# Kernel tuning notes

Hardware: AMD Instinct MI355X
Metric: run time of the kernel (lower is better)

Reference implementation:

```python
import jax, jax.numpy as jnp
import numpy as np

F = 32          # fmap_size = (256 // 16) * 2
WIN = F // 8 - 1  # window = 3
HID = 160
HID4 = 640
N = 4096
Q = 16


def setup_inputs() -> dict:
    key = jax.random.key(0)
    ks = jax.random.split(key, 24)

    def lin(k, i, o):
        return jax.random.normal(k, (i, o), jnp.float32) * (1.0 / np.sqrt(i))

    return {
        "feature_pos": jax.random.normal(ks[0], (N, Q, HID), jnp.float32),
        "query_embedding": jax.random.normal(ks[1], (N, Q, HID), jnp.float32),
        "attn_matrix": jax.random.normal(ks[2], (N, Q, F * F), jnp.float32),
        "ws1": lin(ks[3], HID, HID4), "bs1": jnp.zeros((HID4,), jnp.float32),
        "ws2": lin(ks[4], HID4, HID4), "bs2": jnp.zeros((HID4,), jnp.float32),
        "ws3": lin(ks[5], HID4, HID4), "bs3": jnp.zeros((HID4,), jnp.float32),
        "ws4": lin(ks[6], HID4, 1), "bs4": jnp.zeros((1,), jnp.float32),
        "wp1": lin(ks[7], HID, HID4), "bp1": jnp.zeros((HID4,), jnp.float32),
        "wp2": lin(ks[8], HID4, HID4), "bp2": jnp.zeros((HID4,), jnp.float32),
        "wp3": lin(ks[9], HID4, HID4), "bp3": jnp.zeros((HID4,), jnp.float32),
        "wp4": lin(ks[10], HID4, 4), "bp4": jnp.zeros((4,), jnp.float32),
    }


def _mlp(x, w1, b1, w2, b2, w3, b3, w4, b4):
    h = jax.nn.relu(x @ w1 + b1)
    h = jax.nn.relu(h @ w2 + b2)
    h = jax.nn.relu(h @ w3 + b3)
    return h @ w4 + b4


def _gauss_blur3(x):
    # torchvision GaussianBlur(3, sigma=1.0): separable 3-tap, reflect padding
    e = np.exp(-0.5)
    k = jnp.asarray([e, 1.0, e], jnp.float32) / np.float32(1.0 + 2.0 * e)
    xp = jnp.pad(x, ((0, 0), (1, 1), (0, 0)), mode="reflect")
    x = k[0] * xp[:, :-2] + k[1] * xp[:, 1:-1] + k[2] * xp[:, 2:]
    xp = jnp.pad(x, ((0, 0), (0, 0), (1, 1)), mode="reflect")
    return k[0] * xp[:, :, :-2] + k[1] * xp[:, :, 1:-1] + k[2] * xp[:, :, 2:]


def _process_attnmap(am):
    # am: [N, F, F]
    n = am.shape[0]
    ab = _gauss_blur3(am)
    ab = (ab - ab.mean(axis=(1, 2), keepdims=True)) / jnp.std(ab, axis=(1, 2), keepdims=True, ddof=1)
    idx = jnp.argmax(ab.reshape(n, -1), axis=1)
    px = (idx % F).astype(jnp.int32)
    py = (idx // F).astype(jnp.int32)
    # vectorized windowed mean of clamped sigmoid (masked instead of per-sample slicing)
    s = jnp.clip(jax.nn.sigmoid(am), 1e-4, 1.0 - 1e-4)
    pos = jnp.arange(F)
    colmask = ((pos[None, :] >= jnp.maximum(0, px - WIN)[:, None]) &
               (pos[None, :] < jnp.minimum(F, px + WIN)[:, None])).astype(s.dtype)  # [N,F]
    rowmask = ((pos[None, :] >= jnp.maximum(0, py - WIN)[:, None]) &
               (pos[None, :] < jnp.minimum(F, py + WIN)[:, None])).astype(s.dtype)
    colsum = s.sum(axis=1)  # [N,F] sum over rows -> per-column totals
    rowsum = s.sum(axis=2)  # [N,F] sum over cols -> per-row totals
    tempx = (colsum * colmask).sum(axis=1) / (F * colmask.sum(axis=1))
    tempy = (rowsum * rowmask).sum(axis=1) / (F * rowmask.sum(axis=1))
    prepos = jnp.stack([px, py], axis=1).astype(jnp.float32)          # [N,2]
    presize = jnp.stack([tempx, tempy], axis=1) * np.float32(F)        # [N,2]
    return prepos, presize


def reference(feature_pos, query_embedding, attn_matrix,
              ws1, bs1, ws2, bs2, ws3, bs3, ws4, bs4,
              wp1, bp1, wp2, bp2, wp3, bp3, wp4, bp4):
    n = query_embedding.shape[0]
    qe = query_embedding.mean(axis=1)   # [N, HID]
    fp = feature_pos.mean(axis=1)       # [N, HID]
    am = attn_matrix.mean(axis=1).reshape(n, F, F)
    score = _mlp(qe, ws1, bs1, ws2, bs2, ws3, bs3, ws4, bs4).reshape(n)
    bbox_info = _mlp(fp, wp1, bp1, wp2, bp2, wp3, bp3, wp4, bp4)  # [N,4]
    sizeoffset = jnp.clip(bbox_info[:, :2], -2.0, 2.0)
    posoffset = jnp.clip(bbox_info[:, 2:], -2.0, 2.0)
    prepos, presize = _process_attnmap(am)
    xy = (prepos + posoffset) / np.float32(F)
    wh = (presize + sizeoffset) / np.float32(F)
    xy = xy - 0.5 * wh  # predict_center
    bbox = jnp.concatenate([xy, wh], axis=1)
    return bbox, score
```

## Files before the change

### kernel.cpp

```cpp
#include <hip/hip_runtime.h>
#include <hip/hip_bf16.h>
#include <stdint.h>

#define HID 160
#define HID4 640
#define FDIM 32
#define NPIX 1024

#define GK0 0.27406862f
#define GK1 0.45186276f

typedef __attribute__((ext_vector_type(8))) short short8;
typedef __attribute__((ext_vector_type(4))) float f32x4;

__device__ __forceinline__ ushort f2b(float f) {
  union { float f; uint32_t u; } v; v.f = f;
  uint32_t u = v.u;
  u += 0x7fffu + ((u >> 16) & 1u);
  return (ushort)(u >> 16);
}
__device__ __forceinline__ float b2f(ushort s) {
  union { uint32_t u; float f; } v; v.u = ((uint32_t)s) << 16;
  return v.f;
}

__device__ __forceinline__ void gload16(const ushort* g, ushort* l) {
  __builtin_amdgcn_global_load_lds(
      (const __attribute__((address_space(1))) void*)g,
      (__attribute__((address_space(3))) void*)l, 16, 0, 0);
}

struct AttnSM {
  float am[FDIM][FDIM + 1];
  float tmp[FDIM][FDIM + 1];
  float bl[FDIM][FDIM + 1];
  float rowsum[FDIM], colsum[FDIM];
  float redv[4];
  int redi[4];
};

union GemmSM {
  struct {
    ushort la[2][4096];
    ushort lb[2][2048];
  } g;
  AttnSM a;
};

union PrepSM {
  float t[32][33];
  AttnSM a;
};

__device__ void attn_block(AttnSM& sm, const float* __restrict__ attn,
                           float* __restrict__ pp, int n) {
  const int tid = threadIdx.x;
  const float* base = attn + (size_t)n * (16 * NPIX);
  float4 a = make_float4(0.f, 0.f, 0.f, 0.f);
#pragma unroll
  for (int q = 0; q < 16; ++q) {
    float4 v = *(const float4*)(base + q * NPIX + tid * 4);
    a.x += v.x; a.y += v.y; a.z += v.z; a.w += v.w;
  }
  {
    const int f0 = tid * 4;
    const int r = f0 >> 5, c = f0 & 31;
    sm.am[r][c + 0] = a.x * 0.0625f;
    sm.am[r][c + 1] = a.y * 0.0625f;
    sm.am[r][c + 2] = a.z * 0.0625f;
    sm.am[r][c + 3] = a.w * 0.0625f;
  }
  __syncthreads();
  for (int f = tid; f < NPIX; f += 256) {
    int r = f >> 5, c = f & 31;
    int rm = (r == 0) ? 1 : r - 1;
    int rp = (r == 31) ? 30 : r + 1;
    sm.tmp[r][c] = GK0 * sm.am[rm][c] + GK1 * sm.am[r][c] + GK0 * sm.am[rp][c];
  }
  __syncthreads();
  for (int f = tid; f < NPIX; f += 256) {
    int r = f >> 5, c = f & 31;
    int cm = (c == 0) ? 1 : c - 1;
    int cp = (c == 31) ? 30 : c + 1;
    sm.bl[r][c] = GK0 * sm.tmp[r][cm] + GK1 * sm.tmp[r][c] + GK0 * sm.tmp[r][cp];
  }
  __syncthreads();
  float bv = -1e30f; int bi = 0;
  for (int f = tid; f < NPIX; f += 256) {
    float v = sm.bl[f >> 5][f & 31];
    if (v > bv || (v == bv && f < bi)) { bv = v; bi = f; }
  }
  for (int off = 32; off > 0; off >>= 1) {
    float ov = __shfl_down(bv, off);
    int oi = __shfl_down(bi, off);
    if (ov > bv || (ov == bv && oi < bi)) { bv = ov; bi = oi; }
  }
  if ((tid & 63) == 0) { sm.redv[tid >> 6] = bv; sm.redi[tid >> 6] = bi; }
  for (int f = tid; f < NPIX; f += 256) {
    int r = f >> 5, c = f & 31;
    float s = 1.f / (1.f + expf(-sm.am[r][c]));
    sm.tmp[r][c] = fminf(fmaxf(s, 1e-4f), 0.9999f);
  }
  __syncthreads();
  if (tid < 32) {
    float s = 0.f;
    for (int c = 0; c < 32; ++c) s += sm.tmp[tid][c];
    sm.rowsum[tid] = s;
  } else if (tid < 64) {
    int c = tid - 32;
    float s = 0.f;
    for (int r = 0; r < 32; ++r) s += sm.tmp[r][c];
    sm.colsum[c] = s;
  }
  __syncthreads();
  if (tid == 0) {
    float bestv = sm.redv[0]; int besti = sm.redi[0];
    for (int w = 1; w < 4; ++w)
      if (sm.redv[w] > bestv || (sm.redv[w] == bestv && sm.redi[w] < besti)) {
        bestv = sm.redv[w]; besti = sm.redi[w];
      }
    int px = besti & 31, py = besti >> 5;
    int c0 = max(0, px - 3), c1 = min(32, px + 3);
    float sx = 0.f;
    for (int c = c0; c < c1; ++c) sx += sm.colsum[c];
    float psx = (sx / (32.f * (float)(c1 - c0))) * 32.f;
    int r0 = max(0, py - 3), r1 = min(32, py + 3);
    float sy = 0.f;
    for (int r = r0; r < r1; ++r) sy += sm.rowsum[r];
    float psy = (sy / (32.f * (float)(r1 - r0))) * 32.f;
    pp[n * 4 + 0] = (float)px;
    pp[n * 4 + 1] = (float)py;
    pp[n * 4 + 2] = psx;
    pp[n * 4 + 3] = psy;
  }
}

template <int K>
__global__ __launch_bounds__(256) void gemm_attn(
    const ushort* __restrict__ A0, const ushort* __restrict__ A1,
    const ushort* __restrict__ W0, const ushort* __restrict__ W1,
    const float* __restrict__ B0, const float* __restrict__ B1,
    ushort* __restrict__ O0, ushort* __restrict__ O1,
    const float* __restrict__ attn, float* __restrict__ pp,
    int attn_base, int n_gemm) {
  __shared__ GemmSM sm;
  const int tid = threadIdx.x;

  if ((int)blockIdx.x >= n_gemm) {
    attn_block(sm.a, attn, pp, attn_base + (int)blockIdx.x - n_gemm);
    return;
  }

  const int bid = blockIdx.x;
  const int half = n_gemm >> 1;
  const int chain = bid >= half;
  const int r = chain ? bid - half : bid;
  const int bn = (r % 10) * 64;
  const int bm = (r / 10) * 128;
  const ushort* A = chain ? A1 : A0;
  const ushort* W = chain ? W1 : W0;
  const float* bias = chain ? B1 : B0;
  ushort* O = chain ? O1 : O0;

  const int lane = tid & 63;
  const int wid = tid >> 6;
  const int wr = (wid >> 1) * 64;
  const int wc = (wid & 1) * 32;
  const int l15 = lane & 15;
  const int kq = (lane >> 4) * 8;

  const int rstage = tid >> 2;
  const int cstage = (tid & 3) * 8;
  const int cs_sw = cstage ^ ((rstage & 6) << 2);

  ushort* la = &sm.g.la[0][0];
  ushort* lb = &sm.g.lb[0][0];
  const int ldsw = wid * 512;

  const size_t arow0 = (size_t)(bm + rstage) * K + cs_sw;
  const size_t arow1 = (size_t)(bm + 64 + rstage) * K + cs_sw;
  const size_t brow  = (size_t)(bn + rstage) * K + cs_sw;

  gload16(A + arow0, la + ldsw);
  gload16(A + arow1, la + 2048 + ldsw);
  gload16(W + brow,  lb + ldsw);

  constexpr int NT = K / 32;
  f32x4 acc[4][2] = {};
  for (int t = 0; t < NT; ++t) {
    const int cur = t & 1;
    if (t + 1 < NT) {
      const int k1 = (t + 1) * 32;
      const int nxt = cur ^ 1;
      gload16(A + arow0 + k1, la + nxt * 4096 + ldsw);
      gload16(A + arow1 + k1, la + nxt * 4096 + 2048 + ldsw);
      gload16(W + brow + k1,  lb + nxt * 2048 + ldsw);
      asm volatile("s_waitcnt vmcnt(3)" ::: "memory");
    } else {
      asm volatile("s_waitcnt vmcnt(0)" ::: "memory");
    }
    __builtin_amdgcn_s_barrier();

    const ushort* lac = la + cur * 4096;
    const ushort* lbc = lb + cur * 2048;
    short8 af[4], bf[2];
#pragma unroll
    for (int mi = 0; mi < 4; ++mi) {
      const int rr = wr + mi * 16 + l15;
      af[mi] = *(const short8*)(lac + rr * 32 + (kq ^ ((rr & 6) << 2)));
    }
#pragma unroll
    for (int nj = 0; nj < 2; ++nj) {
      const int rr = wc + nj * 16 + l15;
      bf[nj] = *(const short8*)(lbc + rr * 32 + (kq ^ ((rr & 6) << 2)));
    }
#pragma unroll
    for (int mi = 0; mi < 4; ++mi)
#pragma unroll
      for (int nj = 0; nj < 2; ++nj)
        acc[mi][nj] = __builtin_amdgcn_mfma_f32_16x16x32_bf16(af[mi], bf[nj], acc[mi][nj], 0, 0, 0);

    asm volatile("s_waitcnt lgkmcnt(0)" ::: "memory");
    __builtin_amdgcn_s_barrier();
  }

#pragma unroll
  for (int nj = 0; nj < 2; ++nj) {
    const int col = bn + wc + nj * 16 + l15;
    const float bcol = bias[col];
#pragma unroll
    for (int mi = 0; mi < 4; ++mi) {
      const int rbase = bm + wr + mi * 16 + (lane >> 4) * 4;
#pragma unroll
      for (int b = 0; b < 4; ++b) {
        float v = acc[mi][nj][b] + bcol;
        O[(size_t)(rbase + b) * HID4 + col] = f2b(fmaxf(v, 0.f));
      }
    }
  }
}

__global__ __launch_bounds__(256) void prep_kernel(
    const float* __restrict__ qemb, const float* __restrict__ fpos,
    ushort* __restrict__ qe_b, ushort* __restrict__ fp_b,
    const float* __restrict__ ws1, ushort* __restrict__ wts1,
    const float* __restrict__ wp1, ushort* __restrict__ wtp1,
    const float* __restrict__ ws2, ushort* __restrict__ wts2,
    const float* __restrict__ wp2, ushort* __restrict__ wtp2,
    const float* __restrict__ ws3, ushort* __restrict__ wts3,
    const float* __restrict__ wp3, ushort* __restrict__ wtp3,
    const float* __restrict__ attn, float* __restrict__ pp,
    int n_mean_blocks, int n_trans_blocks, int total) {
  __shared__ PrepSM sm;
  const int tid = threadIdx.x;
  const int bid = blockIdx.x;

  if (bid < n_mean_blocks) {
    int idx = bid * 256 + tid;
    const int pairs = total >> 1;
    const float* src; ushort* dst; int i;
    if (idx < pairs) { src = qemb; dst = qe_b; i = idx; }
    else             { src = fpos; dst = fp_b; i = idx - pairs; }
    int nn = i / (HID / 2);
    int h = (i - nn * (HID / 2)) * 2;
    const float* p = src + (size_t)nn * (16 * HID) + h;
    float sx = 0.f, sy = 0.f;
#pragma unroll
    for (int q = 0; q < 16; ++q) {
      float2 v = *(const float2*)(p + q * HID);
      sx += v.x; sy += v.y;
    }
    ushort2 o;
    o.x = f2b(sx * 0.0625f);
    o.y = f2b(sy * 0.0625f);
    *(ushort2*)(dst + (size_t)nn * HID + h) = o;
    return;
  }

  if (bid < n_mean_blocks + n_trans_blocks) {
    int r = bid - n_mean_blocks;
    const float* in; ushort* out; int K;
    if (r < 100)       { in = ws1; out = wts1; K = HID; }
    else if (r < 200)  { in = wp1; out = wtp1; K = HID; r -= 100; }
    else if (r < 600)  { in = ws2; out = wts2; K = HID4; r -= 200; }
    else if (r < 1000) { in = wp2; out = wtp2; K = HID4; r -= 600; }
    else if (r < 1400) { in = ws3; out = wts3; K = HID4; r -= 1000; }
    else               { in = wp3; out = wtp3; K = HID4; r -= 1400; }
    const int bx = (r % 20) * 32;
    const int by = (r / 20) * 32;
    const int lx = tid & 31;
    const int ly = tid >> 5;
#pragma unroll
    for (int i = 0; i < 4; ++i)
      sm.t[ly + i * 8][lx] = in[(size_t)(by + ly + i * 8) * HID4 + bx + lx];
    __syncthreads();
#pragma unroll
    for (int i = 0; i < 4; ++i)
      out[(size_t)(bx + ly + i * 8) * K + by + lx] = f2b(sm.t[lx][ly + i * 8]);
    return;
  }

  attn_block(sm.a, attn, pp, bid - n_mean_blocks - n_trans_blocks);
}

__global__ __launch_bounds__(256) void final_kernel(
    const ushort* __restrict__ hs, const ushort* __restrict__ hp,
    const float* __restrict__ ws4, const float* __restrict__ bs4,
    const float* __restrict__ wp4, const float* __restrict__ bp4,
    const float* __restrict__ pp, float* __restrict__ out, int N) {
  const int wid = threadIdx.x >> 6;
  const int lane = threadIdx.x & 63;
  const int n = blockIdx.x * 4 + wid;
  if (n >= N) return;
  const ushort* hsr = hs + (size_t)n * HID4;
  const ushort* hpr = hp + (size_t)n * HID4;
  float sc = 0.f, b0 = 0.f, b1 = 0.f, b2 = 0.f, b3 = 0.f;
  for (int j = lane; j < HID4; j += 64) {
    float h1 = b2f(hsr[j]);
    sc += h1 * ws4[j];
    float h2 = b2f(hpr[j]);
    b0 += h2 * wp4[j * 4 + 0];
    b1 += h2 * wp4[j * 4 + 1];
    b2 += h2 * wp4[j * 4 + 2];
    b3 += h2 * wp4[j * 4 + 3];
  }
  for (int off = 32; off > 0; off >>= 1) {
    sc += __shfl_down(sc, off);
    b0 += __shfl_down(b0, off);
    b1 += __shfl_down(b1, off);
    b2 += __shfl_down(b2, off);
    b3 += __shfl_down(b3, off);
  }
  if (lane == 0) {
    sc += bs4[0];
    b0 += bp4[0]; b1 += bp4[1]; b2 += bp4[2]; b3 += bp4[3];
    float so0 = fminf(fmaxf(b0, -2.f), 2.f);
    float so1 = fminf(fmaxf(b1, -2.f), 2.f);
    float po0 = fminf(fmaxf(b2, -2.f), 2.f);
    float po1 = fminf(fmaxf(b3, -2.f), 2.f);
    float px = pp[n * 4 + 0], py = pp[n * 4 + 1];
    float psx = pp[n * 4 + 2], psy = pp[n * 4 + 3];
    float wh0 = (psx + so0) * (1.f / 32.f);
    float wh1 = (psy + so1) * (1.f / 32.f);
    float xy0 = (px + po0) * (1.f / 32.f) - 0.5f * wh0;
    float xy1 = (py + po1) * (1.f / 32.f) - 0.5f * wh1;
    out[n * 4 + 0] = xy0;
    out[n * 4 + 1] = xy1;
    out[n * 4 + 2] = wh0;
    out[n * 4 + 3] = wh1;
    out[(size_t)4 * N + n] = sc;
  }
}

extern "C" void kernel_launch(void* const* d_in, const int* in_sizes, int n_in,
                              void* d_out, int out_size, void* d_ws, size_t ws_size,
                              hipStream_t stream) {
  const float* fpos = (const float*)d_in[0];
  const float* qemb = (const float*)d_in[1];
  const float* attn = (const float*)d_in[2];
  const float* ws1 = (const float*)d_in[3];
  const float* bs1 = (const float*)d_in[4];
  const float* ws2 = (const float*)d_in[5];
  const float* bs2 = (const float*)d_in[6];
  const float* ws3 = (const float*)d_in[7];
  const float* bs3 = (const float*)d_in[8];
  const float* ws4 = (const float*)d_in[9];
  const float* bs4 = (const float*)d_in[10];
  const float* wp1 = (const float*)d_in[11];
  const float* bp1 = (const float*)d_in[12];
  const float* wp2 = (const float*)d_in[13];
  const float* bp2 = (const float*)d_in[14];
  const float* wp3 = (const float*)d_in[15];
  const float* bp3 = (const float*)d_in[16];
  const float* wp4 = (const float*)d_in[17];
  const float* bp4 = (const float*)d_in[18];
  float* out = (float*)d_out;

  const int N = in_sizes[0] / (16 * HID);

  char* ws = (char*)d_ws;
  const size_t SZ_QE = (size_t)N * HID * 2;
  const size_t SZ_W1 = (size_t)HID4 * HID * 2;
  const size_t SZ_W2 = (size_t)HID4 * HID4 * 2;
  const size_t SZ_H  = (size_t)N * HID4 * 2;
  size_t off = 0;
  ushort* qe_b = (ushort*)(ws + off); off += SZ_QE;
  ushort* fp_b = (ushort*)(ws + off); off += SZ_QE;
  ushort* wts1 = (ushort*)(ws + off); off += SZ_W1;
  ushort* wtp1 = (ushort*)(ws + off); off += SZ_W1;
  ushort* wts2 = (ushort*)(ws + off); off += SZ_W2;
  ushort* wtp2 = (ushort*)(ws + off); off += SZ_W2;
  ushort* wts3 = (ushort*)(ws + off); off += SZ_W2;
  ushort* wtp3 = (ushort*)(ws + off); off += SZ_W2;
  ushort* hsA  = (ushort*)(ws + off); off += SZ_H;
  ushort* hsB  = (ushort*)(ws + off); off += SZ_H;
  ushort* hpA  = (ushort*)(ws + off); off += SZ_H;
  ushort* hpB  = (ushort*)(ws + off); off += SZ_H;
  float*  pp   = (float*)(ws + off);  off += (size_t)N * 4 * 4;

  const int a0 = (N * 25) / 64;
  const int a1 = (N * 11) / 64;
  const int a2 = (N * 14) / 64;
  const int a3 = N - a0 - a1 - a2;

  const int total = N * HID;
  const int n_mean = (total + 255) / 256;
  const int n_trans = 1800;
  prep_kernel<<<n_mean + n_trans + a0, 256, 0, stream>>>(
      qemb, fpos, qe_b, fp_b, ws1, wts1, wp1, wtp1, ws2, wts2, wp2, wtp2,
      ws3, wts3, wp3, wtp3, attn, pp, n_mean, n_trans, total);

  const int n_gemm = 2 * (N / 128) * (HID4 / 64);

  gemm_attn<HID><<<n_gemm + a1, 256, 0, stream>>>(
      qe_b, fp_b, wts1, wtp1, bs1, bp1, hsA, hpA, attn, pp, a0, n_gemm);
  gemm_attn<HID4><<<n_gemm + a2, 256, 0, stream>>>(
      hsA, hpA, wts2, wtp2, bs2, bp2, hsB, hpB, attn, pp, a0 + a1, n_gemm);
  gemm_attn<HID4><<<n_gemm + a3, 256, 0, stream>>>(
      hsB, hpB, wts3, wtp3, bs3, bp3, hsA, hpA, attn, pp, a0 + a1 + a2, n_gemm);

  final_kernel<<<(N + 3) / 4, 256, 0, stream>>>(hsA, hpA, ws4, bs4, wp4, bp4, pp, out, N);
}
```

Before: 131.8 us.

## Use 128x128 GEMM tiles with single-stage 160-wide K chunks and rebalance attention blocks

The GEMM tile grows from 128x64 to 128x128, with 4x4 MFMA accumulators per wave. Each step now stages a whole 160-wide K slice into LDS in one shot and does five MFMA sub-steps per barrier. This drops the double-buffered 32-wide pipeline and the XOR swizzle, cutting barriers and reloads of the A tile. The cost is no load/compute overlap, possible LDS bank conflicts from the unswizzled stride-160 layout, and fewer GEMM blocks. Launch-bound occupancy hints are added, and the attention-map blocks are redistributed across the four launches.

```diff
diff --git a/kernel.cpp b/kernel.cpp
--- a/kernel.cpp
+++ b/kernel.cpp
@@ -41,8 +41,8 @@
 
 union GemmSM {
   struct {
-    ushort la[2][4096];
-    ushort lb[2][2048];
+    ushort la[128 * 160];
+    ushort lb[128 * 160];
   } g;
   AttnSM a;
 };
@@ -136,7 +136,7 @@
 }
 
 template <int K>
-__global__ __launch_bounds__(256) void gemm_attn(
+__global__ __launch_bounds__(256, 2) void gemm_attn(
     const ushort* __restrict__ A0, const ushort* __restrict__ A1,
     const ushort* __restrict__ W0, const ushort* __restrict__ W1,
     const float* __restrict__ B0, const float* __restrict__ B1,
@@ -155,8 +155,8 @@
   const int half = n_gemm >> 1;
   const int chain = bid >= half;
   const int r = chain ? bid - half : bid;
-  const int bn = (r % 10) * 64;
-  const int bm = (r / 10) * 128;
+  const int bn = (r % 5) * 128;
+  const int bm = (r / 5) * 128;
   const ushort* A = chain ? A1 : A0;
   const ushort* W = chain ? W1 : W0;
   const float* bias = chain ? B1 : B0;
@@ -165,67 +165,53 @@
   const int lane = tid & 63;
   const int wid = tid >> 6;
   const int wr = (wid >> 1) * 64;
-  const int wc = (wid & 1) * 32;
+  const int wc = (wid & 1) * 64;
   const int l15 = lane & 15;
   const int kq = (lane >> 4) * 8;
 
-  const int rstage = tid >> 2;
-  const int cstage = (tid & 3) * 8;
-  const int cs_sw = cstage ^ ((rstage & 6) << 2);
-
-  ushort* la = &sm.g.la[0][0];
-  ushort* lb = &sm.g.lb[0][0];
-  const int ldsw = wid * 512;
-
-  const size_t arow0 = (size_t)(bm + rstage) * K + cs_sw;
-  const size_t arow1 = (size_t)(bm + 64 + rstage) * K + cs_sw;
-  const size_t brow  = (size_t)(bn + rstage) * K + cs_sw;
-
-  gload16(A + arow0, la + ldsw);
-  gload16(A + arow1, la + 2048 + ldsw);
-  gload16(W + brow,  lb + ldsw);
-
-  constexpr int NT = K / 32;
-  f32x4 acc[4][2] = {};
+  ushort* la = sm.g.la;
+  ushort* lb = sm.g.lb;
+
+  uint offA[10], offB[10];
+#pragma unroll
+  for (int i = 0; i < 10; ++i) {
+    const uint e = (uint)(wid * 10 + i) * 512 + lane * 8;
+    const uint row = e / 160;
+    const uint col = e - row * 160;
+    offA[i] = (uint)(bm + row) * K + col;
+    offB[i] = (uint)(bn + row) * K + col;
+  }
+
+  constexpr int NT = K / 160;
+  f32x4 acc[4][4] = {};
   for (int t = 0; t < NT; ++t) {
-    const int cur = t & 1;
-    if (t + 1 < NT) {
-      const int k1 = (t + 1) * 32;
-      const int nxt = cur ^ 1;
-      gload16(A + arow0 + k1, la + nxt * 4096 + ldsw);
-      gload16(A + arow1 + k1, la + nxt * 4096 + 2048 + ldsw);
-      gload16(W + brow + k1,  lb + nxt * 2048 + ldsw);
-      asm volatile("s_waitcnt vmcnt(3)" ::: "memory");
-    } else {
-      asm volatile("s_waitcnt vmcnt(0)" ::: "memory");
+    const int k0 = t * 160;
+#pragma unroll
+    for (int i = 0; i < 10; ++i) {
+      const int ldso = (wid * 10 + i) * 512;
+      gload16(A + offA[i] + k0, la + ldso);
+      gload16(W + offB[i] + k0, lb + ldso);
     }
-    __builtin_amdgcn_s_barrier();
-
-    const ushort* lac = la + cur * 4096;
-    const ushort* lbc = lb + cur * 2048;
-    short8 af[4], bf[2];
-#pragma unroll
-    for (int mi = 0; mi < 4; ++mi) {
-      const int rr = wr + mi * 16 + l15;
-      af[mi] = *(const short8*)(lac + rr * 32 + (kq ^ ((rr & 6) << 2)));
+    __syncthreads();
+#pragma unroll
+    for (int ks = 0; ks < 5; ++ks) {
+      short8 af[4], bf[4];
+#pragma unroll
+      for (int i = 0; i < 4; ++i) {
+        af[i] = *(const short8*)(la + (wr + i * 16 + l15) * 160 + ks * 32 + kq);
+        bf[i] = *(const short8*)(lb + (wc + i * 16 + l15) * 160 + ks * 32 + kq);
+      }
+#pragma unroll
+      for (int mi = 0; mi < 4; ++mi)
+#pragma unroll
+        for (int nj = 0; nj < 4; ++nj)
+          acc[mi][nj] = __builtin_amdgcn_mfma_f32_16x16x32_bf16(af[mi], bf[nj], acc[mi][nj], 0, 0, 0);
     }
-#pragma unroll
-    for (int nj = 0; nj < 2; ++nj) {
-      const int rr = wc + nj * 16 + l15;
-      bf[nj] = *(const short8*)(lbc + rr * 32 + (kq ^ ((rr & 6) << 2)));
-    }
-#pragma unroll
-    for (int mi = 0; mi < 4; ++mi)
-#pragma unroll
-      for (int nj = 0; nj < 2; ++nj)
-        acc[mi][nj] = __builtin_amdgcn_mfma_f32_16x16x32_bf16(af[mi], bf[nj], acc[mi][nj], 0, 0, 0);
-
-    asm volatile("s_waitcnt lgkmcnt(0)" ::: "memory");
-    __builtin_amdgcn_s_barrier();
-  }
-
-#pragma unroll
-  for (int nj = 0; nj < 2; ++nj) {
+    if (t + 1 < NT) __syncthreads();
+  }
+
+#pragma unroll
+  for (int nj = 0; nj < 4; ++nj) {
     const int col = bn + wc + nj * 16 + l15;
     const float bcol = bias[col];
 #pragma unroll
@@ -240,7 +226,7 @@
   }
 }
 
-__global__ __launch_bounds__(256) void prep_kernel(
+__global__ __launch_bounds__(256, 4) void prep_kernel(
     const float* __restrict__ qemb, const float* __restrict__ fpos,
     ushort* __restrict__ qe_b, ushort* __restrict__ fp_b,
     const float* __restrict__ ws1, ushort* __restrict__ wts1,
@@ -398,10 +384,10 @@
   ushort* hpB  = (ushort*)(ws + off); off += SZ_H;
   float*  pp   = (float*)(ws + off);  off += (size_t)N * 4 * 4;
 
-  const int a0 = (N * 25) / 64;
-  const int a1 = (N * 11) / 64;
-  const int a2 = (N * 14) / 64;
-  const int a3 = N - a0 - a1 - a2;
+  const int a1 = 350;
+  const int a2 = 600;
+  const int a3 = 600;
+  const int a0 = N - a1 - a2 - a3;
 
   const int total = N * HID;
   const int n_mean = (total + 255) / 256;
@@ -410,7 +396,7 @@
       qemb, fpos, qe_b, fp_b, ws1, wts1, wp1, wtp1, ws2, wts2, wp2, wtp2,
       ws3, wts3, wp3, wtp3, attn, pp, n_mean, n_trans, total);
 
-  const int n_gemm = 2 * (N / 128) * (HID4 / 64);
+  const int n_gemm = 2 * (N / 128) * (HID4 / 128);
 
   gemm_attn<HID><<<n_gemm + a1, 256, 0, stream>>>(
       qe_b, fp_b, wts1, wtp1, bs1, bp1, hsA, hpA, attn, pp, a0, n_gemm);
```

Result: faster. 126.4 us (-4.1%).
